# Kernel optimization log

Measured on AMD Instinct MI355X. Metric: run time of the kernel, lower is better.

## Reference

```python
import jax, jax.numpy as jnp
import numpy as np

B, T, I, H, O = 4096, 512, 1, 64, 3

def setup_inputs() -> dict:
    key = jax.random.key(0)
    ks = jax.random.split(key, 7)
    s = 1.0 / np.sqrt(H)  # torch default LSTM init scale
    return {
        "x": jax.random.normal(ks[0], (B, T, I), dtype=jnp.float32),
        "W_ih": jax.random.uniform(ks[1], (4 * H, I), jnp.float32, -s, s),
        "W_hh": jax.random.uniform(ks[2], (4 * H, H), jnp.float32, -s, s),
        "b_ih": jax.random.uniform(ks[3], (4 * H,), jnp.float32, -s, s),
        "b_hh": jax.random.uniform(ks[4], (4 * H,), jnp.float32, -s, s),
        "W_out": jax.random.uniform(ks[5], (O, H), jnp.float32, -s, s),
        "b_out": jax.random.uniform(ks[6], (O,), jnp.float32, -s, s),
    }

def reference(x, W_ih, W_hh, b_ih, b_hh, W_out, b_out):
    # Single-layer LSTM (PyTorch gate order i,f,g,o), zero initial state,
    # then linear head applied to the last hidden state (== r_out[:, -1, :]).
    b = b_ih + b_hh
    Bsz, Hh = x.shape[0], W_hh.shape[1]
    # Precompute input projections for all timesteps: [T, B, 4H]
    x_proj = jnp.einsum('bti,gi->tbg', x, W_ih) + b

    def step(carry, xp_t):
        h, c = carry
        gates = xp_t + h @ W_hh.T  # [B, 4H]
        i, f, g, o = jnp.split(gates, 4, axis=-1)
        c_new = jax.nn.sigmoid(f) * c + jax.nn.sigmoid(i) * jnp.tanh(g)
        h_new = jax.nn.sigmoid(o) * jnp.tanh(c_new)
        return (h_new, c_new), None

    h0 = jnp.zeros((Bsz, Hh), x.dtype)
    (h_last, _), _ = jax.lax.scan(step, (h0, h0), x_proj)
    return h_last @ W_out.T + b_out  # [B, 3]
```

## Files before the change

### kernel.cpp

```cpp
#include <hip/hip_runtime.h>

#define BATCH 4096
#define TT 512
#define HH 64
#define BT 4
#define XS 516
#define HS 72

typedef __attribute__((ext_vector_type(8))) short short8;
typedef __attribute__((ext_vector_type(4))) float floatx4;

__device__ __forceinline__ float sigf(float x) {
    return __builtin_amdgcn_rcpf(1.f + __builtin_amdgcn_exp2f(-1.44269504089f * x));
}
__device__ __forceinline__ float tanhf_(float x) {
    float e = __builtin_amdgcn_exp2f(2.88539008178f * x);
    return 1.f - 2.f * __builtin_amdgcn_rcpf(e + 1.f);
}
__device__ __forceinline__ unsigned short f2bf(float f) {
    unsigned u = __float_as_uint(f);
    u = u + 0x7FFFu + ((u >> 16) & 1u);
    return (unsigned short)(u >> 16);
}

__global__ __launch_bounds__(256, 4) void lstm_kernel(
    const float* __restrict__ x, const float* __restrict__ W_ih,
    const float* __restrict__ W_hh, const float* __restrict__ b_ih,
    const float* __restrict__ b_hh, const float* __restrict__ W_out,
    const float* __restrict__ b_out, float* __restrict__ out)
{
    __shared__ __align__(16) float x_s[BT * XS];
    __shared__ __align__(16) unsigned short hb[2][16 * HS];
    __shared__ __align__(16) float hf[BT * 65];

    const int tid = threadIdx.x;
    const int w = tid >> 6;
    const int l = tid & 63;
    const int q = l >> 4;
    const int c = l & 15;
    const int n = 16 * w + c;
    const int bbase = blockIdx.x * BT;

    for (int i = 0; i < 2; ++i) {
        int flat = i * 256 + tid;
        int row = flat >> 7, c4 = flat & 127;
        const float4* xg = reinterpret_cast<const float4*>(x + (size_t)(bbase + row) * TT);
        float4 v = xg[c4];
        *reinterpret_cast<float4*>(&x_s[row * XS + c4 * 4]) = v;
    }
    for (int i = tid; i < 2 * 16 * HS; i += 256) hb[0][i] = 0;

    short8 bfr[4][2];
    float wih[4], bb[4];
    for (int t = 0; t < 4; ++t) {
        int g = 64 * t + n;
        wih[t] = W_ih[g];
        bb[t] = b_ih[g] + b_hh[g];
        for (int ks = 0; ks < 2; ++ks) {
            const float* wp = W_hh + g * 64 + ks * 32 + q * 8;
            short8 v;
            #pragma unroll
            for (int j = 0; j < 8; ++j) v[j] = (short)f2bf(wp[j]);
            bfr[t][ks] = v;
        }
    }
    float cst = 0.f;

    floatx4 acc[4];
    #pragma unroll
    for (int t = 0; t < 4; ++t) acc[t] = floatx4{0.f, 0.f, 0.f, 0.f};

    __syncthreads();

    int cur = 0;
    for (int ts4 = 0; ts4 < TT; ts4 += 4) {
        float4 xq = *reinterpret_cast<const float4*>(&x_s[q * XS + ts4]);
        #pragma unroll
        for (int u = 0; u < 4; ++u) {
            const unsigned short* hc = hb[cur];
            short8 a0 = *reinterpret_cast<const short8*>(hc + c * HS + q * 8);
            short8 a1 = *reinterpret_cast<const short8*>(hc + c * HS + q * 8 + 32);

            float xv = (&xq.x)[u];
            #pragma unroll
            for (int t = 0; t < 4; ++t) acc[t][0] = fmaf(xv, wih[t], bb[t]);

            #pragma unroll
            for (int t = 0; t < 4; ++t) {
                acc[t] = __builtin_amdgcn_mfma_f32_16x16x32_bf16(a0, bfr[t][0], acc[t], 0, 0, 0);
                acc[t] = __builtin_amdgcn_mfma_f32_16x16x32_bf16(a1, bfr[t][1], acc[t], 0, 0, 0);
            }

            float ig = sigf(acc[0][0]);
            float fg = sigf(acc[1][0]);
            float gv = tanhf_(acc[2][0]);
            float og = sigf(acc[3][0]);
            float cv = fmaf(fg, cst, ig * gv);
            cst = cv;
            float hv = og * tanhf_(cv);
            hb[cur ^ 1][(4 * q) * HS + n] = f2bf(hv);
            if (ts4 + u == TT - 1) hf[q * 65 + n] = hv;
            cur ^= 1;
            __syncthreads();
        }
    }

    if (tid < BT * 3) {
        int row = tid / 3, o = tid % 3;
        float s = b_out[o];
        #pragma unroll 8
        for (int k = 0; k < HH; ++k) s = fmaf(hf[row * 65 + k], W_out[o * 64 + k], s);
        out[(size_t)(bbase + row) * 3 + o] = s;
    }
}

extern "C" void kernel_launch(void* const* d_in, const int* in_sizes, int n_in,
                              void* d_out, int out_size, void* d_ws, size_t ws_size,
                              hipStream_t stream) {
    const float* x     = (const float*)d_in[0];
    const float* W_ih  = (const float*)d_in[1];
    const float* W_hh  = (const float*)d_in[2];
    const float* b_ih  = (const float*)d_in[3];
    const float* b_hh  = (const float*)d_in[4];
    const float* W_out = (const float*)d_in[5];
    const float* b_out = (const float*)d_in[6];
    float* out = (float*)d_out;
    hipLaunchKernelGGL(lstm_kernel, dim3(BATCH / BT), dim3(256), 0, stream,
                       x, W_ih, W_hh, b_ih, b_hh, W_out, b_out, out);
}
```

Baseline: 302.2 us.

## Process 16 batch rows per block using two independent MFMA chains per step

Each block now handles 16 batch rows instead of 4. It packs two rows per MFMA group and runs two independent accumulator chains (hg0/hg1) that interleave activation and matmul, giving the scheduler ILP inside each serial step. The loop is restructured to compute activations first and then sync, load the new h and issue the MFMAs, so there is one barrier per step for 16 rows. The gate math is merged to use fewer reciprocals. This cuts the grid to 256 blocks with launch bounds of 1, so occupancy per CU drops, and the bf16 activation path is unchanged.

```diff
diff --git a/kernel.cpp b/kernel.cpp
--- a/kernel.cpp
+++ b/kernel.cpp
@@ -3,35 +3,28 @@
 #define BATCH 4096
 #define TT 512
 #define HH 64
-#define BT 4
 #define XS 516
 #define HS 72
 
 typedef __attribute__((ext_vector_type(8))) short short8;
 typedef __attribute__((ext_vector_type(4))) float floatx4;
 
-__device__ __forceinline__ float sigf(float x) {
-    return __builtin_amdgcn_rcpf(1.f + __builtin_amdgcn_exp2f(-1.44269504089f * x));
-}
-__device__ __forceinline__ float tanhf_(float x) {
-    float e = __builtin_amdgcn_exp2f(2.88539008178f * x);
-    return 1.f - 2.f * __builtin_amdgcn_rcpf(e + 1.f);
-}
 __device__ __forceinline__ unsigned short f2bf(float f) {
     unsigned u = __float_as_uint(f);
     u = u + 0x7FFFu + ((u >> 16) & 1u);
     return (unsigned short)(u >> 16);
 }
 
-__global__ __launch_bounds__(256, 4) void lstm_kernel(
+__global__ __launch_bounds__(256, 1) void lstm_kernel(
     const float* __restrict__ x, const float* __restrict__ W_ih,
     const float* __restrict__ W_hh, const float* __restrict__ b_ih,
     const float* __restrict__ b_hh, const float* __restrict__ W_out,
     const float* __restrict__ b_out, float* __restrict__ out)
 {
-    __shared__ __align__(16) float x_s[BT * XS];
-    __shared__ __align__(16) unsigned short hb[2][16 * HS];
-    __shared__ __align__(16) float hf[BT * 65];
+    __shared__ __align__(16) float x_s[16 * XS];
+    __shared__ __align__(16) unsigned short hg0[2][16 * HS];
+    __shared__ __align__(16) unsigned short hg1[2][16 * HS];
+    __shared__ __align__(16) float hf[16 * 65];
 
     const int tid = threadIdx.x;
     const int w = tid >> 6;
@@ -39,16 +32,16 @@
     const int q = l >> 4;
     const int c = l & 15;
     const int n = 16 * w + c;
-    const int bbase = blockIdx.x * BT;
+    const int bbase = blockIdx.x * 16;
 
-    for (int i = 0; i < 2; ++i) {
+    for (int i = 0; i < 8; ++i) {
         int flat = i * 256 + tid;
         int row = flat >> 7, c4 = flat & 127;
         const float4* xg = reinterpret_cast<const float4*>(x + (size_t)(bbase + row) * TT);
         float4 v = xg[c4];
         *reinterpret_cast<float4*>(&x_s[row * XS + c4 * 4]) = v;
     }
-    for (int i = tid; i < 2 * 16 * HS; i += 256) hb[0][i] = 0;
+    for (int i = tid; i < 2 * 16 * HS; i += 256) { (&hg0[0][0])[i] = 0; (&hg1[0][0])[i] = 0; }
 
     short8 bfr[4][2];
     float wih[4], bb[4];
@@ -64,54 +57,95 @@
             bfr[t][ks] = v;
         }
     }
-    float cst = 0.f;
 
-    floatx4 acc[4];
+    float cs0[2] = {0.f, 0.f}, cs1[2] = {0.f, 0.f};
+    float hv0[2], hv1[2];
+
+    floatx4 ac0[4], ac1[4];
     #pragma unroll
-    for (int t = 0; t < 4; ++t) acc[t] = floatx4{0.f, 0.f, 0.f, 0.f};
+    for (int t = 0; t < 4; ++t) { ac0[t] = floatx4{0.f,0.f,0.f,0.f}; ac1[t] = floatx4{0.f,0.f,0.f,0.f}; }
+
+    const int aoff = c * HS + q * 8;
+    const int woff = (4 * q) * HS + n;
+    const float* xr0 = &x_s[(2 * q) * XS];
+    const float* xr1 = &x_s[(8 + 2 * q) * XS];
+    const float L1 = 1.44269504089f;
+    const float L2 = 2.88539008178f;
 
     __syncthreads();
 
-    int cur = 0;
-    for (int ts4 = 0; ts4 < TT; ts4 += 4) {
-        float4 xq = *reinterpret_cast<const float4*>(&x_s[q * XS + ts4]);
+    {
+        float a0 = xr0[0], a1 = xr0[XS], b0 = xr1[0], b1 = xr1[XS];
         #pragma unroll
-        for (int u = 0; u < 4; ++u) {
-            const unsigned short* hc = hb[cur];
-            short8 a0 = *reinterpret_cast<const short8*>(hc + c * HS + q * 8);
-            short8 a1 = *reinterpret_cast<const short8*>(hc + c * HS + q * 8 + 32);
-
-            float xv = (&xq.x)[u];
-            #pragma unroll
-            for (int t = 0; t < 4; ++t) acc[t][0] = fmaf(xv, wih[t], bb[t]);
-
-            #pragma unroll
-            for (int t = 0; t < 4; ++t) {
-                acc[t] = __builtin_amdgcn_mfma_f32_16x16x32_bf16(a0, bfr[t][0], acc[t], 0, 0, 0);
-                acc[t] = __builtin_amdgcn_mfma_f32_16x16x32_bf16(a1, bfr[t][1], acc[t], 0, 0, 0);
-            }
-
-            float ig = sigf(acc[0][0]);
-            float fg = sigf(acc[1][0]);
-            float gv = tanhf_(acc[2][0]);
-            float og = sigf(acc[3][0]);
-            float cv = fmaf(fg, cst, ig * gv);
-            cst = cv;
-            float hv = og * tanhf_(cv);
-            hb[cur ^ 1][(4 * q) * HS + n] = f2bf(hv);
-            if (ts4 + u == TT - 1) hf[q * 65 + n] = hv;
-            cur ^= 1;
-            __syncthreads();
+        for (int t = 0; t < 4; ++t) {
+            ac0[t][0] = fmaf(a0, wih[t], bb[t]); ac0[t][1] = fmaf(a1, wih[t], bb[t]);
+            ac1[t][0] = fmaf(b0, wih[t], bb[t]); ac1[t][1] = fmaf(b1, wih[t], bb[t]);
         }
     }
 
-    if (tid < BT * 3) {
+    #define ACT(ACC, CST, HV) do {                                              \
+        _Pragma("unroll")                                                       \
+        for (int rr = 0; rr < 2; ++rr) {                                        \
+            float gi = ACC[0][rr], gf = ACC[1][rr], gg = ACC[2][rr], go = ACC[3][rr]; \
+            float ei = __builtin_amdgcn_exp2f(-L1 * gi);                        \
+            float ef = __builtin_amdgcn_exp2f(-L1 * gf);                        \
+            float eg = __builtin_amdgcn_exp2f( L2 * gg);                        \
+            float eo = __builtin_amdgcn_exp2f(-L1 * go);                        \
+            float pf1 = 1.f + ef, pig = (1.f + ei) * (1.f + eg);                \
+            float num = fmaf(CST[rr], pig, (eg - 1.f) * pf1);                   \
+            CST[rr] = num * __builtin_amdgcn_rcpf(pf1 * pig);                   \
+            float ec = __builtin_amdgcn_exp2f(L2 * CST[rr]);                    \
+            HV[rr] = (ec - 1.f) * __builtin_amdgcn_rcpf((1.f + eo) * (1.f + ec)); \
+        } } while (0)
+
+    for (int k = 0; k < TT - 1; ++k) {
+        unsigned short* d0 = hg0[k & 1];
+        unsigned short* d1 = hg1[k & 1];
+
+        ACT(ac0, cs0, hv0);
+        d0[woff] = f2bf(hv0[0]); d0[woff + HS] = f2bf(hv0[1]);
+        ACT(ac1, cs1, hv1);
+        d1[woff] = f2bf(hv1[0]); d1[woff + HS] = f2bf(hv1[1]);
+
+        __syncthreads();
+
+        short8 a00 = *reinterpret_cast<const short8*>(d0 + aoff);
+        short8 a01 = *reinterpret_cast<const short8*>(d0 + aoff + 32);
+        short8 a10 = *reinterpret_cast<const short8*>(d1 + aoff);
+        short8 a11 = *reinterpret_cast<const short8*>(d1 + aoff + 32);
+
+        float xa0 = xr0[k + 1], xa1 = xr0[XS + k + 1];
+        float xb0 = xr1[k + 1], xb1 = xr1[XS + k + 1];
+        #pragma unroll
+        for (int t = 0; t < 4; ++t) {
+            ac0[t][0] = fmaf(xa0, wih[t], bb[t]); ac0[t][1] = fmaf(xa1, wih[t], bb[t]);
+            ac1[t][0] = fmaf(xb0, wih[t], bb[t]); ac1[t][1] = fmaf(xb1, wih[t], bb[t]);
+        }
+        #pragma unroll
+        for (int t = 0; t < 4; ++t) {
+            ac0[t] = __builtin_amdgcn_mfma_f32_16x16x32_bf16(a00, bfr[t][0], ac0[t], 0, 0, 0);
+            ac0[t] = __builtin_amdgcn_mfma_f32_16x16x32_bf16(a01, bfr[t][1], ac0[t], 0, 0, 0);
+            ac1[t] = __builtin_amdgcn_mfma_f32_16x16x32_bf16(a10, bfr[t][0], ac1[t], 0, 0, 0);
+            ac1[t] = __builtin_amdgcn_mfma_f32_16x16x32_bf16(a11, bfr[t][1], ac1[t], 0, 0, 0);
+        }
+    }
+
+    ACT(ac0, cs0, hv0);
+    ACT(ac1, cs1, hv1);
+    hf[(2 * q) * 65 + n] = hv0[0];
+    hf[(2 * q + 1) * 65 + n] = hv0[1];
+    hf[(8 + 2 * q) * 65 + n] = hv1[0];
+    hf[(8 + 2 * q + 1) * 65 + n] = hv1[1];
+    __syncthreads();
+
+    if (tid < 16 * 3) {
         int row = tid / 3, o = tid % 3;
         float s = b_out[o];
         #pragma unroll 8
         for (int k = 0; k < HH; ++k) s = fmaf(hf[row * 65 + k], W_out[o * 64 + k], s);
         out[(size_t)(bbase + row) * 3 + o] = s;
     }
+    #undef ACT
 }
 
 extern "C" void kernel_launch(void* const* d_in, const int* in_sizes, int n_in,
@@ -125,6 +159,6 @@
     const float* W_out = (const float*)d_in[5];
     const float* b_out = (const float*)d_in[6];
     float* out = (float*)d_out;
-    hipLaunchKernelGGL(lstm_kernel, dim3(BATCH / BT), dim3(256), 0, stream,
+    hipLaunchKernelGGL(lstm_kernel, dim3(BATCH / 16), dim3(256), 0, stream,
                        x, W_ih, W_hh, b_ih, b_hh, W_out, b_out, out);
 }
```

After: 393.5 us. 1.3x slower.
